# Optimization experiments

Hardware: AMD Instinct MI355X
Metric: run time of the kernel (lower is better)

The kernel has to match this reference:

```python
import jax, jax.numpy as jnp
import numpy as np

EPS = 1e-4

def softmax_kernel(data, proj, is_query):
    # FAVOR+ positive softmax random features; data: [b,h,l,d], proj: [d,m]
    d = data.shape[-1]
    m = proj.shape[-1]
    data_normalizer = d ** -0.25  # normalize_data=True
    ratio = m ** -0.5
    data_dash = jnp.einsum('bhld,dm->bhlm', data, proj) * data_normalizer
    diag = 0.5 * jnp.sum(data * data, axis=-1, keepdims=True) * (data_normalizer ** 2)
    if is_query:
        stab = jnp.max(data_dash, axis=-1, keepdims=True)   # per-token max
    else:
        stab = jnp.max(data_dash, axis=(-2, -1), keepdims=True)  # per (b,h) max
    out = ratio * (jnp.exp(data_dash - diag - stab) + EPS)
    return out, stab

def low_mem_attn(qp, kp, v, causal, chunk):
    # qp,kp: [b,h,l,m] positive features; v: [b,h,l,d]
    b, h, l, m = qp.shape
    d = v.shape[-1]
    if not causal:
        kv = jnp.einsum('bhlm,bhld->bhmd', kp, v)
        den = jnp.einsum('bhlm,bhm->bhl', qp, jnp.sum(kp, axis=2))
        return jnp.einsum('bhlm,bhmd->bhld', qp, kv) / den[..., None]
    nc = l // chunk
    qc = qp.reshape(b, h, nc, chunk, m)
    kc = kp.reshape(b, h, nc, chunk, m)
    vc = v.reshape(b, h, nc, chunk, d)
    # intra-chunk causal part
    mask = jnp.tril(jnp.ones((chunk, chunk), dtype=qp.dtype))
    scores = jnp.einsum('bhcim,bhcjm->bhcij', qc, kc) * mask
    intra = jnp.einsum('bhcij,bhcjd->bhcid', scores, vc)
    intra_den = jnp.sum(scores, axis=-1)  # [b,h,nc,chunk]
    # inter-chunk via exclusive cumulative sums of KV state
    kv = jnp.einsum('bhcjm,bhcjd->bhcmd', kc, vc)          # per-chunk KV
    kv_prev = jnp.cumsum(kv, axis=2) - kv                   # exclusive cumsum
    ks = jnp.sum(kc, axis=3)                                # [b,h,nc,m]
    ks_prev = jnp.cumsum(ks, axis=2) - ks
    inter = jnp.einsum('bhcim,bhcmd->bhcid', qc, kv_prev)
    inter_den = jnp.einsum('bhcim,bhcm->bhci', qc, ks_prev)
    out = (intra + inter) / (intra_den + inter_den)[..., None]
    return out.reshape(b, h, l, d)


def setup_inputs() -> dict:
    key = jax.random.key(0)
    k1, k2, k3, k4 = jax.random.split(key, 4)
    B, H, L, D, M = 2, 16, 4096, 64, 64
    return {
        'q': jax.random.normal(k1, (B, H, L, D), dtype=jnp.float32),
        'k': jax.random.normal(k2, (B, H, L, D), dtype=jnp.float32),
        'v': jax.random.normal(k3, (B, H, L, D), dtype=jnp.float32),
        'projection_matrix': jax.random.normal(k4, (D, M), dtype=jnp.float32),
        'chunk_size': 128,
    }


def reference(q, k, v, projection_matrix, chunk_size):
    qp, _ = softmax_kernel(q, projection_matrix, is_query=True)
    kp, _key_maxima = softmax_kernel(k, projection_matrix, is_query=False)
    o = low_mem_attn(qp, kp, v, causal=True, chunk=chunk_size)
    return o
```

## Files before the change

### kernel.cpp

```cpp
#include <hip/hip_runtime.h>
#include <hip/hip_bf16.h>

#define TPB 256
#define ATPB 512

constexpr int   Bc = 2, Hc = 16, Lc = 4096, Dc = 64, Mc = 64, CHc = 128;
constexpr int   NCc = Lc / CHc;
constexpr int   BHc = Bc * Hc;
constexpr float DNF    = 0.35355339059327373f;
constexpr float RATIOF = 0.125f;
constexpr float EPSF   = 1e-4f;

constexpr long QP_OFF  = 0;
constexpr long KP_OFF  = 4194304;
constexpr long KPB_OFF = 12582912;
constexpr long VTB_OFF = 16777216;
constexpr long KV_OFF  = 20971520;
constexpr long KVB_OFF = 25165824;
constexpr long KS_OFF  = 27262976;
constexpr long HM_OFF  = 27328512;

typedef __attribute__((ext_vector_type(8))) short bf16x8;
typedef __attribute__((ext_vector_type(4))) float f32x4;

__device__ __forceinline__ unsigned fordmap(float f) {
  unsigned u = __float_as_uint(f);
  return (u & 0x80000000u) ? ~u : (u | 0x80000000u);
}
__device__ __forceinline__ float fordunmap(unsigned u) {
  return __uint_as_float((u & 0x80000000u) ? (u & 0x7fffffffu) : ~u);
}
__device__ __forceinline__ unsigned pk2(float a, float b) {
  union { __hip_bfloat16 h; unsigned short u; } ca, cb;
  ca.h = __float2bfloat16(a); cb.h = __float2bfloat16(b);
  return ((unsigned)cb.u << 16) | (unsigned)ca.u;
}
__device__ __forceinline__ short f2bf(float a) {
  union { __hip_bfloat16 h; short s; } c; c.h = __float2bfloat16(a); return c.s;
}
__device__ __forceinline__ float bf2f(short s) {
  return __uint_as_float(((unsigned)(unsigned short)s) << 16);
}

__global__ void k_init(unsigned* hmax) {
  int t = threadIdx.x;
  if (t < BHc) hmax[t] = 0u;
}

template <bool IS_Q>
__global__ __launch_bounds__(TPB) void k_feat(const float* __restrict__ x,
                                              const float* __restrict__ P,
                                              float* __restrict__ outf,
                                              short* __restrict__ outb,
                                              unsigned* __restrict__ hmax) {
  __shared__ short xb[128 * 72];
  __shared__ short Pt[64 * 72];
  __shared__ float od[128 * 68];
  __shared__ float diag_s[128];
  __shared__ unsigned bmax_s;
  const int t = threadIdx.x;
  const long rowbase = (long)blockIdx.x * 128;
  for (int i = t; i < 4096; i += TPB) {
    const int r = i >> 5, d2 = (i & 31) * 2;
    float2 xv = *(const float2*)&x[rowbase * 64 + r * 64 + d2];
    *(unsigned*)&xb[r * 72 + d2] = pk2(xv.x, xv.y);
  }
  for (int i = t; i < 4096; i += TPB) {
    const int d = i >> 6, m = i & 63;
    Pt[m * 72 + d] = f2bf(P[i]);
  }
  if (t == 0) bmax_s = 0u;
  {
    const int row = t >> 1, half = t & 1;
    float s = 0.f;
#pragma unroll
    for (int d = 0; d < 32; d += 4) {
      float4 vv = *(const float4*)&x[(rowbase + row) * 64 + half * 32 + d];
      s += vv.x * vv.x + vv.y * vv.y + vv.z * vv.z + vv.w * vv.w;
    }
    s += __shfl_xor(s, 1);
    if (half == 0) diag_s[row] = 0.0625f * s;
  }
  __syncthreads();

  const int w = t >> 6, lane = t & 63;
  const int lrow = lane & 15, quad = lane >> 4;
  float tmax = -1e30f;
#pragma unroll
  for (int rt2 = 0; rt2 < 2; ++rt2) {
    const int rt = w * 2 + rt2;
    const bf16x8 a0 = *(const bf16x8*)&xb[(rt * 16 + lrow) * 72 + quad * 8];
    const bf16x8 a1 = *(const bf16x8*)&xb[(rt * 16 + lrow) * 72 + 32 + quad * 8];
    f32x4 c[4];
#pragma unroll
    for (int ct = 0; ct < 4; ++ct) {
      const bf16x8 b0 = *(const bf16x8*)&Pt[(ct * 16 + lrow) * 72 + quad * 8];
      const bf16x8 b1 = *(const bf16x8*)&Pt[(ct * 16 + lrow) * 72 + 32 + quad * 8];
      f32x4 cc = {0.f, 0.f, 0.f, 0.f};
      cc = __builtin_amdgcn_mfma_f32_16x16x32_bf16(a0, b0, cc, 0, 0, 0);
      cc = __builtin_amdgcn_mfma_f32_16x16x32_bf16(a1, b1, cc, 0, 0, 0);
#pragma unroll
      for (int r = 0; r < 4; ++r) cc[r] *= DNF;
      c[ct] = cc;
    }
    if constexpr (IS_Q) {
      short* ob = (short*)od;
#pragma unroll
      for (int r = 0; r < 4; ++r) {
        float mx = fmaxf(fmaxf(c[0][r], c[1][r]), fmaxf(c[2][r], c[3][r]));
#pragma unroll
        for (int off = 1; off < 16; off <<= 1) mx = fmaxf(mx, __shfl_xor(mx, off));
        const int row = rt * 16 + quad * 4 + r;
        const float dg = diag_s[row];
#pragma unroll
        for (int ct = 0; ct < 4; ++ct)
          ob[row * 64 + ct * 16 + lrow] =
              f2bf(RATIOF * (expf(c[ct][r] - dg - mx) + EPSF));
      }
    } else {
#pragma unroll
      for (int r = 0; r < 4; ++r) {
        const int row = rt * 16 + quad * 4 + r;
        const float dg = diag_s[row];
#pragma unroll
        for (int ct = 0; ct < 4; ++ct) {
          tmax = fmaxf(tmax, c[ct][r]);
          od[row * 68 + ct * 16 + lrow] = c[ct][r] - dg;
        }
      }
    }
  }
  if constexpr (!IS_Q) {
#pragma unroll
    for (int off = 1; off < 64; off <<= 1) tmax = fmaxf(tmax, __shfl_xor(tmax, off));
    if (lane == 0) atomicMax(&bmax_s, fordmap(tmax));
  }
  __syncthreads();
  if constexpr (IS_Q) {
    const short* ob = (const short*)od;
    for (int i = t; i < 1024; i += TPB)
      *(uint4*)&outb[rowbase * 64 + i * 8] = *(const uint4*)&ob[i * 8];
  } else {
    for (int i = t; i < 2048; i += TPB) {
      const int row = i >> 4, c4 = (i & 15) * 4;
      *(float4*)&outf[rowbase * 64 + row * 64 + c4] = *(const float4*)&od[row * 68 + c4];
    }
    if (t == 0) atomicMax(&hmax[rowbase >> 12], bmax_s);
  }
}

__global__ __launch_bounds__(TPB) void k_ckv(const float* __restrict__ kp,
                                             const float* __restrict__ v,
                                             float* __restrict__ kvT,
                                             float* __restrict__ ks,
                                             short* __restrict__ kpb,
                                             short* __restrict__ vtb,
                                             const unsigned* __restrict__ hmax) {
  __shared__ float kps[128 * 68];
  __shared__ float vs[128 * 68];
  const int t = threadIdx.x;
  const int bhc = blockIdx.x;
  const long base = (long)bhc * 8192;
  const float stab = fordunmap(hmax[bhc >> 5]);
  for (int i = t; i < 8192; i += TPB) {
    int r = i >> 6, d = i & 63;
    kps[r * 68 + d] = RATIOF * (expf(kp[base + i] - stab) + EPSF);
    vs[r * 68 + d]  = v[base + i];
  }
  __syncthreads();
  for (int i = t; i < 2048; i += TPB) {
    const int r = i >> 4, c4 = (i & 15) * 4;
    float4 kk = *(const float4*)&kps[r * 68 + c4];
    uint2 pk; pk.x = pk2(kk.x, kk.y); pk.y = pk2(kk.z, kk.w);
    *(uint2*)&kpb[base + r * 64 + c4] = pk;
  }
  for (int i = t; i < 4096; i += TPB) {
    const int jp = i & 63, d = i >> 6;
    *(unsigned*)&vtb[base + d * 128 + 2 * jp] =
        pk2(vs[(2 * jp) * 68 + d], vs[(2 * jp + 1) * 68 + d]);
  }
  const int dd = t & 31, mg = t >> 5;
  const int d0 = dd * 2, m0 = mg * 8;
  float a0[8], a1[8];
#pragma unroll
  for (int i = 0; i < 8; ++i) { a0[i] = 0.f; a1[i] = 0.f; }
  for (int j = 0; j < 128; ++j) {
    float2 vv = *(const float2*)&vs[j * 68 + d0];
    float4 k0 = *(const float4*)&kps[j * 68 + m0];
    float4 k1 = *(const float4*)&kps[j * 68 + m0 + 4];
    a0[0] += vv.x * k0.x; a0[1] += vv.x * k0.y; a0[2] += vv.x * k0.z; a0[3] += vv.x * k0.w;
    a0[4] += vv.x * k1.x; a0[5] += vv.x * k1.y; a0[6] += vv.x * k1.z; a0[7] += vv.x * k1.w;
    a1[0] += vv.y * k0.x; a1[1] += vv.y * k0.y; a1[2] += vv.y * k0.z; a1[3] += vv.y * k0.w;
    a1[4] += vv.y * k1.x; a1[5] += vv.y * k1.y; a1[6] += vv.y * k1.z; a1[7] += vv.y * k1.w;
  }
  const long kvb = (long)bhc * 4096;
  *(float4*)&kvT[kvb + (long)d0 * 64 + m0]           = make_float4(a0[0], a0[1], a0[2], a0[3]);
  *(float4*)&kvT[kvb + (long)d0 * 64 + m0 + 4]       = make_float4(a0[4], a0[5], a0[6], a0[7]);
  *(float4*)&kvT[kvb + (long)(d0 + 1) * 64 + m0]     = make_float4(a1[0], a1[1], a1[2], a1[3]);
  *(float4*)&kvT[kvb + (long)(d0 + 1) * 64 + m0 + 4] = make_float4(a1[4], a1[5], a1[6], a1[7]);
  if (t < 64) {
    float s = 0.f;
    for (int j = 0; j < 128; ++j) s += kps[j * 68 + t];
    ks[bhc * 64 + t] = s;
  }
}

__global__ void k_scan_kv(const float* __restrict__ kv, short* __restrict__ kvb) {
  const int tid = blockIdx.x * TPB + threadIdx.x;
  const int bh = tid >> 12, rem = tid & 4095;
  float run = 0.f;
  for (int c = 0; c < NCc; ++c) {
    const long idx = ((long)(bh * NCc + c)) * 4096 + rem;
    kvb[idx] = f2bf(run);
    run += kv[idx];
  }
}

__global__ void k_scan_ks(float* __restrict__ ks) {
  const int tid = blockIdx.x * TPB + threadIdx.x;
  if (tid >= BHc * 64) return;
  const int bh = tid >> 6, m = tid & 63;
  float run = 0.f;
  for (int c = 0; c < NCc; ++c) {
    const int idx = (bh * NCc + c) * 64 + m;
    const float val = ks[idx];
    ks[idx] = run;
    run += val;
  }
}

__global__ __launch_bounds__(ATPB, 4) void k_attn(const short* __restrict__ qpb,
                                                  const short* __restrict__ kpb,
                                                  const short* __restrict__ vtb,
                                                  const short* __restrict__ kvb,
                                                  const float* __restrict__ ksp,
                                                  float* __restrict__ outp) {
  __shared__ short Ks[128 * 72];
  __shared__ short Vt[64 * 136];
  __shared__ short KVt[64 * 72];
  __shared__ short Ps[128 * 136];
  __shared__ float kss[64];
  __shared__ float dens[128];
  const int t = threadIdx.x;
  const int bhc = blockIdx.x;
  const long cbase = (long)bhc * 8192;

  for (int i = t; i < 1024; i += ATPB) {
    const int r = i >> 3, c8 = (i & 7) * 8;
    *(uint4*)&Ks[r * 72 + c8] = *(const uint4*)&kpb[cbase + r * 64 + c8];
  }
  for (int i = t; i < 1024; i += ATPB) {
    const int d = i >> 4, c8 = (i & 15) * 8;
    *(uint4*)&Vt[d * 136 + c8] = *(const uint4*)&vtb[cbase + d * 128 + c8];
  }
  {
    const int d = t >> 3, c8 = (t & 7) * 8;
    *(uint4*)&KVt[d * 72 + c8] = *(const uint4*)&kvb[(long)bhc * 4096 + d * 64 + c8];
  }
  if (t < 64) kss[t] = ksp[bhc * 64 + t];
  for (int i = t; i < 1024; i += ATPB) {
    const int tp = i >> 8, rr = (i >> 4) & 15, cc = i & 15;
    Ps[(tp * 32 + rr) * 136 + tp * 32 + 16 + cc] = 0;
  }
  const int w = t >> 6, lane = t & 63;
  const int lrow = lane & 15, quad = lane >> 4;
  const int ri = w;
  const long qrb = cbase + (long)(ri * 16 + lrow) * 64;
  const bf16x8 a0 = *(const bf16x8*)&qpb[qrb + quad * 8];
  const bf16x8 a1 = *(const bf16x8*)&qpb[qrb + 32 + quad * 8];
  __syncthreads();

  float qks = 0.f;
#pragma unroll
  for (int j = 0; j < 8; ++j) {
    qks += bf2f(a0[j]) * kss[quad * 8 + j];
    qks += bf2f(a1[j]) * kss[32 + quad * 8 + j];
  }
  qks += __shfl_xor(qks, 16);
  qks += __shfl_xor(qks, 32);
  if (quad == 0) dens[ri * 16 + lrow] = qks;

  float rs0 = 0.f, rs1 = 0.f, rs2 = 0.f, rs3 = 0.f;
  for (int cj = 0; cj <= ri; ++cj) {
    const bf16x8 b0 = *(const bf16x8*)&Ks[(cj * 16 + lrow) * 72 + quad * 8];
    const bf16x8 b1 = *(const bf16x8*)&Ks[(cj * 16 + lrow) * 72 + 32 + quad * 8];
    f32x4 c = {0.f, 0.f, 0.f, 0.f};
    c = __builtin_amdgcn_mfma_f32_16x16x32_bf16(a0, b0, c, 0, 0, 0);
    c = __builtin_amdgcn_mfma_f32_16x16x32_bf16(a1, b1, c, 0, 0, 0);
    if (cj == ri) {
#pragma unroll
      for (int r = 0; r < 4; ++r)
        if (lrow > quad * 4 + r) c[r] = 0.f;
    }
    const int colb = cj * 16 + lrow;
    Ps[(ri * 16 + quad * 4 + 0) * 136 + colb] = f2bf(c[0]); rs0 += c[0];
    Ps[(ri * 16 + quad * 4 + 1) * 136 + colb] = f2bf(c[1]); rs1 += c[1];
    Ps[(ri * 16 + quad * 4 + 2) * 136 + colb] = f2bf(c[2]); rs2 += c[2];
    Ps[(ri * 16 + quad * 4 + 3) * 136 + colb] = f2bf(c[3]); rs3 += c[3];
  }
#pragma unroll
  for (int off = 1; off < 16; off <<= 1) {
    rs0 += __shfl_xor(rs0, off);
    rs1 += __shfl_xor(rs1, off);
    rs2 += __shfl_xor(rs2, off);
    rs3 += __shfl_xor(rs3, off);
  }
  if (lrow == 0) {
    dens[ri * 16 + quad * 4 + 0] += rs0;
    dens[ri * 16 + quad * 4 + 1] += rs1;
    dens[ri * 16 + quad * 4 + 2] += rs2;
    dens[ri * 16 + quad * 4 + 3] += rs3;
  }

  f32x4 acc0 = {0.f,0.f,0.f,0.f}, acc1 = {0.f,0.f,0.f,0.f};
  f32x4 acc2 = {0.f,0.f,0.f,0.f}, acc3 = {0.f,0.f,0.f,0.f};
  const int nj = (ri + 2) >> 1;
  for (int jc = 0; jc < nj; ++jc) {
    const bf16x8 a  = *(const bf16x8*)&Ps[(ri * 16 + lrow) * 136 + jc * 32 + quad * 8];
    const bf16x8 b0 = *(const bf16x8*)&Vt[(lrow) * 136 + jc * 32 + quad * 8];
    const bf16x8 b1 = *(const bf16x8*)&Vt[(16 + lrow) * 136 + jc * 32 + quad * 8];
    const bf16x8 b2 = *(const bf16x8*)&Vt[(32 + lrow) * 136 + jc * 32 + quad * 8];
    const bf16x8 b3 = *(const bf16x8*)&Vt[(48 + lrow) * 136 + jc * 32 + quad * 8];
    acc0 = __builtin_amdgcn_mfma_f32_16x16x32_bf16(a, b0, acc0, 0, 0, 0);
    acc1 = __builtin_amdgcn_mfma_f32_16x16x32_bf16(a, b1, acc1, 0, 0, 0);
    acc2 = __builtin_amdgcn_mfma_f32_16x16x32_bf16(a, b2, acc2, 0, 0, 0);
    acc3 = __builtin_amdgcn_mfma_f32_16x16x32_bf16(a, b3, acc3, 0, 0, 0);
  }
  {
    const bf16x8 b0 = *(const bf16x8*)&KVt[(lrow) * 72 + quad * 8];
    const bf16x8 b1 = *(const bf16x8*)&KVt[(16 + lrow) * 72 + quad * 8];
    const bf16x8 b2 = *(const bf16x8*)&KVt[(32 + lrow) * 72 + quad * 8];
    const bf16x8 b3 = *(const bf16x8*)&KVt[(48 + lrow) * 72 + quad * 8];
    acc0 = __builtin_amdgcn_mfma_f32_16x16x32_bf16(a0, b0, acc0, 0, 0, 0);
    acc1 = __builtin_amdgcn_mfma_f32_16x16x32_bf16(a0, b1, acc1, 0, 0, 0);
    acc2 = __builtin_amdgcn_mfma_f32_16x16x32_bf16(a0, b2, acc2, 0, 0, 0);
    acc3 = __builtin_amdgcn_mfma_f32_16x16x32_bf16(a0, b3, acc3, 0, 0, 0);
    const bf16x8 c0 = *(const bf16x8*)&KVt[(lrow) * 72 + 32 + quad * 8];
    const bf16x8 c1 = *(const bf16x8*)&KVt[(16 + lrow) * 72 + 32 + quad * 8];
    const bf16x8 c2 = *(const bf16x8*)&KVt[(32 + lrow) * 72 + 32 + quad * 8];
    const bf16x8 c3 = *(const bf16x8*)&KVt[(48 + lrow) * 72 + 32 + quad * 8];
    acc0 = __builtin_amdgcn_mfma_f32_16x16x32_bf16(a1, c0, acc0, 0, 0, 0);
    acc1 = __builtin_amdgcn_mfma_f32_16x16x32_bf16(a1, c1, acc1, 0, 0, 0);
    acc2 = __builtin_amdgcn_mfma_f32_16x16x32_bf16(a1, c2, acc2, 0, 0, 0);
    acc3 = __builtin_amdgcn_mfma_f32_16x16x32_bf16(a1, c3, acc3, 0, 0, 0);
  }
#pragma unroll
  for (int r = 0; r < 4; ++r) {
    const int row = ri * 16 + quad * 4 + r;
    const float inv = 1.f / dens[row];
    const long ob = cbase + (long)row * 64 + lrow;
    outp[ob]      = acc0[r] * inv;
    outp[ob + 16] = acc1[r] * inv;
    outp[ob + 32] = acc2[r] * inv;
    outp[ob + 48] = acc3[r] * inv;
  }
}

extern "C" void kernel_launch(void* const* d_in, const int* in_sizes, int n_in,
                              void* d_out, int out_size, void* d_ws, size_t ws_size,
                              hipStream_t stream) {
  const float* q = (const float*)d_in[0];
  const float* k = (const float*)d_in[1];
  const float* v = (const float*)d_in[2];
  const float* P = (const float*)d_in[3];
  float* ws = (float*)d_ws;
  short*    qpb  = (short*)(ws + QP_OFF);
  float*    kp   = ws + KP_OFF;
  short*    kpb  = (short*)(ws + KPB_OFF);
  short*    vtb  = (short*)(ws + VTB_OFF);
  float*    kvT  = ws + KV_OFF;
  short*    kvb  = (short*)(ws + KVB_OFF);
  float*    ks   = ws + KS_OFF;
  unsigned* hmax = (unsigned*)(ws + HM_OFF);
  float* out = (float*)d_out;

  k_init<<<1, 64, 0, stream>>>(hmax);
  k_feat<true><<<dim3(1024), dim3(TPB), 0, stream>>>(q, P, nullptr, qpb, nullptr);
  k_feat<false><<<dim3(1024), dim3(TPB), 0, stream>>>(k, P, kp, nullptr, hmax);
  k_ckv<<<dim3(1024), dim3(TPB), 0, stream>>>(kp, v, kvT, ks, kpb, vtb, hmax);
  k_scan_kv<<<dim3(512), dim3(TPB), 0, stream>>>(kvT, kvb);
  k_scan_ks<<<dim3(8), dim3(TPB), 0, stream>>>(ks);
  k_attn<<<dim3(1024), dim3(ATPB), 0, stream>>>(qpb, kpb, vtb, kvb, ks, out);
}
```

Measured before the change: 224.9 us.

## Use bf16 MFMA for per-chunk KV in k_ckv and merge scan kernels

Rewrites the per-chunk KV outer-product kernel to stage transposed bf16 K and V features in shared memory and compute the 64x64 KV block with 16x16x32 bf16 MFMA instructions instead of scalar fp32 FMAs. The column sums of K are folded into the load loop using shared-memory atomics. The two scan kernels are merged into one launch, with the last block handling the K-sum scan. This cuts ALU work and one launch, but the chunk KV state is now accumulated from bf16-rounded inputs, which lowers precision.

```diff
diff --git a/kernel.cpp b/kernel.cpp
--- a/kernel.cpp
+++ b/kernel.cpp
@@ -156,76 +156,90 @@
                                              short* __restrict__ kpb,
                                              short* __restrict__ vtb,
                                              const unsigned* __restrict__ hmax) {
-  __shared__ float kps[128 * 68];
-  __shared__ float vs[128 * 68];
+  __shared__ short Kt[64 * 136];
+  __shared__ short Vt[64 * 136];
+  __shared__ float ks_s[64];
   const int t = threadIdx.x;
   const int bhc = blockIdx.x;
   const long base = (long)bhc * 8192;
   const float stab = fordunmap(hmax[bhc >> 5]);
-  for (int i = t; i < 8192; i += TPB) {
-    int r = i >> 6, d = i & 63;
-    kps[r * 68 + d] = RATIOF * (expf(kp[base + i] - stab) + EPSF);
-    vs[r * 68 + d]  = v[base + i];
-  }
-  __syncthreads();
-  for (int i = t; i < 2048; i += TPB) {
-    const int r = i >> 4, c4 = (i & 15) * 4;
-    float4 kk = *(const float4*)&kps[r * 68 + c4];
-    uint2 pk; pk.x = pk2(kk.x, kk.y); pk.y = pk2(kk.z, kk.w);
-    *(uint2*)&kpb[base + r * 64 + c4] = pk;
-  }
-  for (int i = t; i < 4096; i += TPB) {
-    const int jp = i & 63, d = i >> 6;
-    *(unsigned*)&vtb[base + d * 128 + 2 * jp] =
-        pk2(vs[(2 * jp) * 68 + d], vs[(2 * jp + 1) * 68 + d]);
-  }
-  const int dd = t & 31, mg = t >> 5;
-  const int d0 = dd * 2, m0 = mg * 8;
-  float a0[8], a1[8];
-#pragma unroll
-  for (int i = 0; i < 8; ++i) { a0[i] = 0.f; a1[i] = 0.f; }
-  for (int j = 0; j < 128; ++j) {
-    float2 vv = *(const float2*)&vs[j * 68 + d0];
-    float4 k0 = *(const float4*)&kps[j * 68 + m0];
-    float4 k1 = *(const float4*)&kps[j * 68 + m0 + 4];
-    a0[0] += vv.x * k0.x; a0[1] += vv.x * k0.y; a0[2] += vv.x * k0.z; a0[3] += vv.x * k0.w;
-    a0[4] += vv.x * k1.x; a0[5] += vv.x * k1.y; a0[6] += vv.x * k1.z; a0[7] += vv.x * k1.w;
-    a1[0] += vv.y * k0.x; a1[1] += vv.y * k0.y; a1[2] += vv.y * k0.z; a1[3] += vv.y * k0.w;
-    a1[4] += vv.y * k1.x; a1[5] += vv.y * k1.y; a1[6] += vv.y * k1.z; a1[7] += vv.y * k1.w;
+  if (t < 64) ks_s[t] = 0.f;
+  __syncthreads();
+  {
+    const int m2 = (t & 31) * 2;
+    float s0 = 0.f, s1 = 0.f;
+    for (int i = t; i < 4096; i += TPB) {
+      const int j = i >> 5;
+      float2 kk = *(const float2*)&kp[base + j * 64 + m2];
+      const float e0 = RATIOF * (expf(kk.x - stab) + EPSF);
+      const float e1 = RATIOF * (expf(kk.y - stab) + EPSF);
+      *(unsigned*)&kpb[base + j * 64 + m2] = pk2(e0, e1);
+      Kt[m2 * 136 + j] = f2bf(e0);
+      Kt[(m2 + 1) * 136 + j] = f2bf(e1);
+      s0 += e0; s1 += e1;
+    }
+    atomicAdd(&ks_s[m2], s0);
+    atomicAdd(&ks_s[m2 + 1], s1);
+  }
+  {
+    const int d2 = (t & 31) * 2;
+    for (int i = t; i < 4096; i += TPB) {
+      const int j = i >> 5;
+      float2 vv = *(const float2*)&v[base + j * 64 + d2];
+      Vt[d2 * 136 + j] = f2bf(vv.x);
+      Vt[(d2 + 1) * 136 + j] = f2bf(vv.y);
+    }
+  }
+  __syncthreads();
+  for (int i = t; i < 1024; i += TPB) {
+    const int d = i >> 4, c8 = (i & 15) * 8;
+    *(uint4*)&vtb[base + d * 128 + c8] = *(const uint4*)&Vt[d * 136 + c8];
+  }
+  if (t < 64) ks[bhc * 64 + t] = ks_s[t];
+  const int w = t >> 6, lane = t & 63;
+  const int lrow = lane & 15, quad = lane >> 4;
+  f32x4 acc[4];
+#pragma unroll
+  for (int mt = 0; mt < 4; ++mt) acc[mt] = (f32x4){0.f, 0.f, 0.f, 0.f};
+#pragma unroll
+  for (int ksq = 0; ksq < 4; ++ksq) {
+    const bf16x8 a = *(const bf16x8*)&Vt[(w * 16 + lrow) * 136 + ksq * 32 + quad * 8];
+#pragma unroll
+    for (int mt = 0; mt < 4; ++mt) {
+      const bf16x8 b = *(const bf16x8*)&Kt[(mt * 16 + lrow) * 136 + ksq * 32 + quad * 8];
+      acc[mt] = __builtin_amdgcn_mfma_f32_16x16x32_bf16(a, b, acc[mt], 0, 0, 0);
+    }
   }
   const long kvb = (long)bhc * 4096;
-  *(float4*)&kvT[kvb + (long)d0 * 64 + m0]           = make_float4(a0[0], a0[1], a0[2], a0[3]);
-  *(float4*)&kvT[kvb + (long)d0 * 64 + m0 + 4]       = make_float4(a0[4], a0[5], a0[6], a0[7]);
-  *(float4*)&kvT[kvb + (long)(d0 + 1) * 64 + m0]     = make_float4(a1[0], a1[1], a1[2], a1[3]);
-  *(float4*)&kvT[kvb + (long)(d0 + 1) * 64 + m0 + 4] = make_float4(a1[4], a1[5], a1[6], a1[7]);
-  if (t < 64) {
-    float s = 0.f;
-    for (int j = 0; j < 128; ++j) s += kps[j * 68 + t];
-    ks[bhc * 64 + t] = s;
-  }
-}
-
-__global__ void k_scan_kv(const float* __restrict__ kv, short* __restrict__ kvb) {
-  const int tid = blockIdx.x * TPB + threadIdx.x;
-  const int bh = tid >> 12, rem = tid & 4095;
-  float run = 0.f;
-  for (int c = 0; c < NCc; ++c) {
-    const long idx = ((long)(bh * NCc + c)) * 4096 + rem;
-    kvb[idx] = f2bf(run);
-    run += kv[idx];
-  }
-}
-
-__global__ void k_scan_ks(float* __restrict__ ks) {
-  const int tid = blockIdx.x * TPB + threadIdx.x;
-  if (tid >= BHc * 64) return;
-  const int bh = tid >> 6, m = tid & 63;
-  float run = 0.f;
-  for (int c = 0; c < NCc; ++c) {
-    const int idx = (bh * NCc + c) * 64 + m;
-    const float val = ks[idx];
-    ks[idx] = run;
-    run += val;
+#pragma unroll
+  for (int mt = 0; mt < 4; ++mt)
+#pragma unroll
+    for (int r = 0; r < 4; ++r)
+      kvT[kvb + (long)(w * 16 + quad * 4 + r) * 64 + mt * 16 + lrow] = acc[mt][r];
+}
+
+__global__ void k_scan(const float* __restrict__ kv, short* __restrict__ kvb,
+                       float* __restrict__ ks) {
+  if (blockIdx.x < 512) {
+    const int tid = blockIdx.x * TPB + threadIdx.x;
+    const int bh = tid >> 12, rem = tid & 4095;
+    float run = 0.f;
+    for (int c = 0; c < NCc; ++c) {
+      const long idx = ((long)(bh * NCc + c)) * 4096 + rem;
+      kvb[idx] = f2bf(run);
+      run += kv[idx];
+    }
+  } else {
+    for (int tid = threadIdx.x; tid < BHc * 64; tid += TPB) {
+      const int bh = tid >> 6, m = tid & 63;
+      float run = 0.f;
+      for (int c = 0; c < NCc; ++c) {
+        const int idx = (bh * NCc + c) * 64 + m;
+        const float val = ks[idx];
+        ks[idx] = run;
+        run += val;
+      }
+    }
   }
 }
 
@@ -378,7 +392,6 @@
   k_feat<true><<<dim3(1024), dim3(TPB), 0, stream>>>(q, P, nullptr, qpb, nullptr);
   k_feat<false><<<dim3(1024), dim3(TPB), 0, stream>>>(k, P, kp, nullptr, hmax);
   k_ckv<<<dim3(1024), dim3(TPB), 0, stream>>>(kp, v, kvT, ks, kpb, vtb, hmax);
-  k_scan_kv<<<dim3(512), dim3(TPB), 0, stream>>>(kvT, kvb);
-  k_scan_ks<<<dim3(8), dim3(TPB), 0, stream>>>(ks);
+  k_scan<<<dim3(513), dim3(TPB), 0, stream>>>(kvT, kvb, ks);
   k_attn<<<dim3(1024), dim3(ATPB), 0, stream>>>(qpb, kpb, vtb, kvb, ks, out);
 }
```

New measurement: 213.4 us. -5.1%, faster.
